# Kernel tuning notes

Measured on AMD Instinct MI355X. Metric: run time of the kernel, lower is better.

Reference implementation:

```python
import jax, jax.numpy as jnp
import numpy as np

B, T, C, H = 4, 2048, 1024, 16
HD = C // H  # head dim = 64

def setup_inputs() -> dict:
    key = jax.random.key(0)
    k1, k2, k3 = jax.random.split(key, 3)
    x = jax.random.normal(k1, (B, T, C), dtype=jnp.float32)
    w_attn = jax.random.normal(k2, (C, 3 * C), dtype=jnp.float32) * 0.02
    w_proj = jax.random.normal(k3, (C, C), dtype=jnp.float32) * 0.02
    return {"x": x, "w_attn": w_attn, "w_proj": w_proj}

def reference(x, w_attn, w_proj):
    b, t, c = x.shape
    qkv = x @ w_attn  # [B,T,3C]
    q, k, v = jnp.split(qkv, 3, axis=-1)
    # [B,T,C] -> [B,H,T,HD]
    def heads(z):
        return z.reshape(b, t, H, HD).transpose(0, 2, 1, 3)
    q, k, v = heads(q), heads(k), heads(v)
    scale = 1.0 / jnp.sqrt(jnp.float32(HD))
    att = jnp.einsum('bhqd,bhkd->bhqk', q, k) * scale  # [B,H,T,T]
    causal = jnp.tril(jnp.ones((t, t), dtype=bool))
    att = jnp.where(causal[None, None], att, -jnp.inf)
    att = jax.nn.softmax(att, axis=-1)
    y = jnp.einsum('bhqk,bhkd->bhqd', att, v)  # [B,H,T,HD]
    y = y.transpose(0, 2, 1, 3).reshape(b, t, c)
    return y @ w_proj
```

## Files before the change

### kernel.cpp

```cpp
#include <hip/hip_runtime.h>
#include <hip/hip_bf16.h>

typedef short bf16x8 __attribute__((ext_vector_type(8)));
typedef short short4v __attribute__((ext_vector_type(4)));
typedef float f32x4 __attribute__((ext_vector_type(4)));
typedef float f32x16 __attribute__((ext_vector_type(16)));

template <bool V> struct BoolC { static constexpr bool value = V; };

__device__ __forceinline__ short f2b(float f) {
  __hip_bfloat16 h = __float2bfloat16(f);
  union { __hip_bfloat16 h; short s; } u; u.h = h; return u.s;
}

__device__ __forceinline__ unsigned cvtpk_bf16(float lo, float hi) {
  unsigned r;
  asm("v_cvt_pk_bf16_f32 %0, %1, %2" : "=v"(r) : "v"(lo), "v"(hi));
  return r;
}

__device__ __forceinline__ f32x16 mfma32(bf16x8 a, bf16x8 b, f32x16 c) {
  return __builtin_amdgcn_mfma_f32_32x32x16_bf16(a, b, c, 0, 0, 0);
}

template <int N> __device__ __forceinline__ void vmwait() {
  if constexpr (N == 0) asm volatile("s_waitcnt vmcnt(0)" ::: "memory");
  else if constexpr (N == 1) asm volatile("s_waitcnt vmcnt(1)" ::: "memory");
  else if constexpr (N == 2) asm volatile("s_waitcnt vmcnt(2)" ::: "memory");
  else if constexpr (N == 3) asm volatile("s_waitcnt vmcnt(3)" ::: "memory");
  else if constexpr (N == 4) asm volatile("s_waitcnt vmcnt(4)" ::: "memory");
  else if constexpr (N == 5) asm volatile("s_waitcnt vmcnt(5)" ::: "memory");
  else if constexpr (N == 6) asm volatile("s_waitcnt vmcnt(6)" ::: "memory");
  else if constexpr (N == 7) asm volatile("s_waitcnt vmcnt(7)" ::: "memory");
  else asm volatile("s_waitcnt vmcnt(8)" ::: "memory");
}

__device__ __forceinline__ void async_copy16(const short* g, short* l) {
  __builtin_amdgcn_global_load_lds((const __attribute__((address_space(1))) void*)g,
                                   (__attribute__((address_space(3))) void*)l, 16, 0, 0);
}

__global__ __launch_bounds__(256) void pre_kernel(const float* __restrict__ x, short* __restrict__ xb,
                                                  const float* __restrict__ wa, short* __restrict__ waT,
                                                  const float* __restrict__ wp, short* __restrict__ wpT,
                                                  float qscale) {
  const int tid = threadIdx.x;
  const int blk = blockIdx.x;
  if (blk < 8192) {
    const int i = blk * 256 + tid;
    const float4 v = ((const float4*)x)[i];
    short4v o;
    o[0] = f2b(v.x); o[1] = f2b(v.y); o[2] = f2b(v.z); o[3] = f2b(v.w);
    ((short4v*)xb)[i] = o;
    return;
  }
  __shared__ float t[32][33];
  const float* in; short* out;
  int idx, gxb, Cn, qrows; float qs;
  if (blk < 11264) { idx = blk - 8192;  in = wa; out = waT; gxb = 96; Cn = 3072; qrows = 1024; qs = qscale; }
  else             { idx = blk - 11264; in = wp; out = wpT; gxb = 32; Cn = 1024; qrows = 0;    qs = 1.0f; }
  const int bx = idx % gxb, by = idx / gxb;
  const int tx = tid & 31, ty = tid >> 5;
  const int c0 = bx * 32, r0 = by * 32;
#pragma unroll
  for (int yy = 0; yy < 32; yy += 8)
    t[ty + yy][tx] = in[(size_t)(r0 + ty + yy) * Cn + (c0 + tx)];
  __syncthreads();
#pragma unroll
  for (int yy = 0; yy < 32; yy += 8) {
    const int orow = c0 + ty + yy;
    float v = t[tx][ty + yy];
    if (orow < qrows) v *= qs;
    out[(size_t)orow * 1024 + (r0 + tx)] = f2b(v);
  }
}

__global__ __launch_bounds__(256) void vtrans_kernel(const short* __restrict__ qkv,
                                                     short* __restrict__ vT) {
  constexpr int T = 2048, C3 = 3072, HD = 64;
  const int bh = blockIdx.y, b = bh >> 4, h = bh & 15;
  const int t0 = blockIdx.x * 64;
  __shared__ short tile[64][72];
  const int tid = threadIdx.x;
  const int tr = tid >> 2, dc = (tid & 3) * 16;
  const short* src = qkv + (size_t)b * T * C3 + (size_t)(t0 + tr) * C3 + 2048 + h * HD + dc;
  *(bf16x8*)&tile[tr][dc] = *(const bf16x8*)src;
  *(bf16x8*)&tile[tr][dc + 8] = *(const bf16x8*)(src + 8);
  __syncthreads();
  const int dr = tid >> 2, tc = (tid & 3) * 16;
  bf16x8 o0, o1;
#pragma unroll
  for (int i = 0; i < 8; i++) o0[i] = tile[tc + i][dr];
#pragma unroll
  for (int i = 0; i < 8; i++) o1[i] = tile[tc + 8 + i][dr];
  short* dst = vT + ((size_t)bh * HD + dr) * T + t0 + tc;
  *(bf16x8*)dst = o0;
  *(bf16x8*)(dst + 8) = o1;
}

template <int BN, typename OutT>
__global__ __launch_bounds__(256, 2) void gemm2b_kernel(const short* __restrict__ A,
                                                        const short* __restrict__ Bt,
                                                        OutT* __restrict__ C,
                                                        int M, int N, int K) {
  constexpr int NB = BN / 64;
  constexpr int NBU = BN / 32;
  constexpr int NSTREAM = NBU + 4;
  __shared__ short ldsA[2][128 * 64];
  __shared__ short ldsB[2][BN * 64];

  const int tid = threadIdx.x;
  const int w = tid >> 6, lane = tid & 63;
  const int quad = lane >> 4, l16 = lane & 15;
  const int wn = w * (BN / 4);

  const int gx = gridDim.x;
  const int nwg = gx * gridDim.y;
  const int flat = blockIdx.y * gx + blockIdx.x;
  const int swz = (flat & 7) * (nwg >> 3) + (flat >> 3);
  const int bn = swz % gx, bm = swz / gx;
  const int m0 = bm * 128, n0 = bn * BN;

  const int rsub = lane >> 3;
  const int cl = (lane & 7) ^ rsub;
  const short* pAsrc = A + (size_t)(m0 + w * 8 + rsub) * K + cl * 8;
  const short* pBsrc = Bt + (size_t)(n0 + w * 8 + rsub) * K + cl * 8;

  f32x4 acc[8][NB] = {};
  bf16x8 bfr[NB][2];

  auto issue = [&](int i, int buf, int tt) {
    if (i < NBU)
      async_copy16(pBsrc + (size_t)(i * 32) * K + tt * 64, &ldsB[buf][(i * 32 + w * 8) * 64]);
    else
      async_copy16(pAsrc + (size_t)((i - NBU) * 32) * K + tt * 64,
                   &ldsA[buf][((i - NBU) * 32 + w * 8) * 64]);
  };
  auto readA = [&](bf16x8 (&af)[2][2], int buf, int P) {
#pragma unroll
    for (int mm = 0; mm < 2; ++mm)
#pragma unroll
      for (int kh = 0; kh < 2; ++kh)
        af[mm][kh] = *(const bf16x8*)&ldsA[buf][(P * 32 + mm * 16 + l16) * 64 +
                                                (((kh * 4 + quad) ^ (l16 & 7)) * 8)];
  };
  auto readB = [&](int buf) {
#pragma unroll
    for (int nf = 0; nf < NB; ++nf)
#pragma unroll
      for (int kh = 0; kh < 2; ++kh)
        bfr[nf][kh] = *(const bf16x8*)&ldsB[buf][(wn + nf * 16 + l16) * 64 +
                                                 (((kh * 4 + quad) ^ (l16 & 7)) * 8)];
  };

#define PHASE(P)                                                                               \
  {                                                                                            \
    constexpr int ISS0 = (NSTREAM + 3) >> 2, ISS1 = (NSTREAM + 2) >> 2,                        \
                  ISS2 = (NSTREAM + 1) >> 2;                                                   \
    constexpr int CUM = ((P) > 0 ? ISS0 : 0) + ((P) > 1 ? ISS1 : 0) + ((P) > 2 ? ISS2 : 0);    \
    constexpr int GS = NSTREAM - (NBU + 1 + (P)) + CUM;                                        \
    constexpr int GL = 3 - (P);                                                                \
    if constexpr ((P) == 0) asm volatile("s_waitcnt lgkmcnt(0)" ::: "memory");                 \
    if constexpr (LAST) vmwait<GL>(); else vmwait<GS>();                                       \
    __builtin_amdgcn_s_barrier();                                                              \
    bf16x8 af[2][2];                                                                           \
    readA(af, buf, (P));                                                                       \
    if constexpr ((P) == 0) readB(buf);                                                        \
    if constexpr (!LAST) {                                                                     \
      constexpr int NI = (NSTREAM + 3 - (P)) >> 2;                                             \
      _Pragma("unroll") for (int ii = 0; ii < NI; ++ii) issue(CUM + ii, buf ^ 1, t + 1);       \
    }                                                                                          \
    __builtin_amdgcn_s_setprio(1);                                                             \
    _Pragma("unroll") for (int mm = 0; mm < 2; ++mm)                                           \
    _Pragma("unroll") for (int nf = 0; nf < NB; ++nf) {                                        \
      acc[(P)*2 + mm][nf] = __builtin_amdgcn_mfma_f32_16x16x32_bf16(af[mm][0], bfr[nf][0],     \
                                                                    acc[(P)*2 + mm][nf], 0, 0, 0); \
      acc[(P)*2 + mm][nf] = __builtin_amdgcn_mfma_f32_16x16x32_bf16(af[mm][1], bfr[nf][1],     \
                                                                    acc[(P)*2 + mm][nf], 0, 0, 0); \
    }                                                                                          \
    __builtin_amdgcn_s_setprio(0);                                                             \
  }

#pragma unroll
  for (int i = 0; i < NSTREAM; ++i) issue(i, 0, 0);

  const int NT = K >> 6;
  auto tile = [&](int t, int buf, auto lastc) {
    constexpr bool LAST = decltype(lastc)::value;
    PHASE(0)
    PHASE(1)
    PHASE(2)
    PHASE(3)
  };
  for (int t = 0; t < NT - 1; ++t) tile(t, t & 1, BoolC<false>{});
  tile(NT - 1, (NT - 1) & 1, BoolC<true>{});
#undef PHASE

  (void)M;
#pragma unroll
  for (int mf = 0; mf < 8; ++mf)
#pragma unroll
    for (int nf = 0; nf < NB; ++nf) {
      const int col = n0 + wn + nf * 16 + l16;
#pragma unroll
      for (int r = 0; r < 4; ++r) {
        const int row = m0 + mf * 16 + quad * 4 + r;
        if constexpr (sizeof(OutT) == 4)
          C[(size_t)row * N + col] = acc[mf][nf][r];
        else
          C[(size_t)row * N + col] = f2b(acc[mf][nf][r]);
      }
    }
}

__global__ __launch_bounds__(256, 2) void attn_kernel(const short* __restrict__ qkv,
                                                      const short* __restrict__ vT,
                                                      short* __restrict__ y) {
  constexpr int T = 2048, C3 = 3072, Cc = 1024, HD = 64;
  const int f = blockIdx.y * 8 + blockIdx.x;
  const int bh = (f & 7) * 8 + ((f >> 3) & 7);
  const int xb = f >> 6;
  const int b = bh >> 4, h = bh & 15;
  const int tid = threadIdx.x, lane = tid & 63, wave = tid >> 6;
  const int l32 = lane & 31, hi = lane >> 5;

  __shared__ short Ksb[2][64 * 64];
  __shared__ short Vtb[2][64 * 64];

  const size_t base = (size_t)b * T * C3;
  const int qcol = h * HD, kcol = Cc + h * HD;
  const size_t vtbase = (size_t)bh * HD * T;

  const int r8 = lane >> 3;
  const int cg8 = ((lane & 7) ^ r8) * 8;
  const short* gk[2];
  const short* gv[2];
  short* lk[2][2]; short* lv[2][2];
#pragma unroll
  for (int t8 = 0; t8 < 2; t8++) {
    const int row = wave * 16 + t8 * 8 + r8;
    gk[t8] = qkv + base + (size_t)row * C3 + kcol + cg8;
    gv[t8] = vT + vtbase + (size_t)row * T + cg8;
#pragma unroll
    for (int bu = 0; bu < 2; bu++) {
      lk[bu][t8] = &Ksb[bu][(wave * 16 + t8 * 8) * 64];
      lv[bu][t8] = &Vtb[bu][(wave * 16 + t8 * 8) * 64];
    }
  }
  const int rs7 = l32 & 7;

  bf16x8 ones;
#pragma unroll
  for (int i = 0; i < 8; i++) ones[i] = (short)0x3F80;

  for (int half = 0; half < 2; half++) {
    const int t = half ? xb : (15 - xb);
    const int q0 = t * 128;
    const int jmax = 2 * t + 1;
    const int jd = 2 * t + (wave >> 1);
    const int qrow = q0 + wave * 32 + l32;

    bf16x8 qf[4];
    {
      const short* qp = qkv + base + (size_t)qrow * C3 + qcol + hi * 8;
#pragma unroll
      for (int wk = 0; wk < 4; wk++) qf[wk] = *(const bf16x8*)(qp + wk * 16);
    }

    f32x16 o0 = {}, o1 = {}, lC = {};

    async_copy16(gk[0], lk[0][0]);
    async_copy16(gk[1], lk[0][1]);
    async_copy16(gv[0], lv[0][0]);
    async_copy16(gv[1], lv[0][1]);

    for (int j = 0; j <= jmax; j++) {
      const int cur = j & 1;
      __syncthreads();

      if (j < jmax) {
        const size_t ko = (size_t)(j + 1) * 64 * C3;
        const int vo = (j + 1) * 64;
        async_copy16(gk[0] + ko, lk[cur ^ 1][0]);
        async_copy16(gk[1] + ko, lk[cur ^ 1][1]);
        async_copy16(gv[0] + vo, lv[cur ^ 1][0]);
        async_copy16(gv[1] + vo, lv[cur ^ 1][1]);
      }

      if (j > jd) continue;

      const bool up = (64 * j + 32) <= (q0 + wave * 32 + 31);

      f32x16 st0 = {}, st1 = {};
      __builtin_amdgcn_s_setprio(1);
#pragma unroll
      for (int wk = 0; wk < 4; wk++) {
        const bf16x8 k0 = *(const bf16x8*)&Ksb[cur][l32 * 64 + (((2 * wk + hi) ^ rs7) * 8)];
        st0 = mfma32(k0, qf[wk], st0);
      }
      if (up) {
#pragma unroll
        for (int wk = 0; wk < 4; wk++) {
          const bf16x8 k1 = *(const bf16x8*)&Ksb[cur][(32 + l32) * 64 + (((2 * wk + hi) ^ rs7) * 8)];
          st1 = mfma32(k1, qf[wk], st1);
        }
      }
      __builtin_amdgcn_s_setprio(0);

      if (j == jd) {
#pragma unroll
        for (int r = 0; r < 16; r++) {
          const int kvl = 64 * j + (r & 3) + 8 * (r >> 2) + 4 * hi;
          if (kvl > qrow) st0[r] = -INFINITY;
          if (up && (kvl + 32 > qrow)) st1[r] = -INFINITY;
        }
      }

      bf16x8 vf00, vf01, vf10, vf11, vf02, vf03, vf12, vf13;
      vf00 = *(const bf16x8*)&Vtb[cur][l32 * 64 + (((0 + hi) ^ rs7) * 8)];
      vf01 = *(const bf16x8*)&Vtb[cur][l32 * 64 + (((2 + hi) ^ rs7) * 8)];
      vf10 = *(const bf16x8*)&Vtb[cur][(32 + l32) * 64 + (((0 + hi) ^ rs7) * 8)];
      vf11 = *(const bf16x8*)&Vtb[cur][(32 + l32) * 64 + (((2 + hi) ^ rs7) * 8)];
      if (up) {
        vf02 = *(const bf16x8*)&Vtb[cur][l32 * 64 + (((4 + hi) ^ rs7) * 8)];
        vf03 = *(const bf16x8*)&Vtb[cur][l32 * 64 + (((6 + hi) ^ rs7) * 8)];
        vf12 = *(const bf16x8*)&Vtb[cur][(32 + l32) * 64 + (((4 + hi) ^ rs7) * 8)];
        vf13 = *(const bf16x8*)&Vtb[cur][(32 + l32) * 64 + (((6 + hi) ^ rs7) * 8)];
      }

#pragma unroll
      for (int r = 0; r < 16; r++) st0[r] = __builtin_amdgcn_exp2f(st0[r]);
      bf16x8 pa0, pa1, pa2, pa3;
      {
        unsigned a0 = cvtpk_bf16(st0[0], st0[1]), c0 = cvtpk_bf16(st0[2], st0[3]);
        unsigned b0 = cvtpk_bf16(st0[4], st0[5]), d0 = cvtpk_bf16(st0[6], st0[7]);
        asm volatile("v_permlane32_swap_b32 %0, %1" : "+v"(a0), "+v"(b0));
        asm volatile("v_permlane32_swap_b32 %0, %1" : "+v"(c0), "+v"(d0));
        union { unsigned u[4]; bf16x8 v; } p; p.u[0] = a0; p.u[1] = c0; p.u[2] = b0; p.u[3] = d0;
        pa0 = p.v;
        unsigned a1 = cvtpk_bf16(st0[8], st0[9]), c1 = cvtpk_bf16(st0[10], st0[11]);
        unsigned b1 = cvtpk_bf16(st0[12], st0[13]), d1 = cvtpk_bf16(st0[14], st0[15]);
        asm volatile("v_permlane32_swap_b32 %0, %1" : "+v"(a1), "+v"(b1));
        asm volatile("v_permlane32_swap_b32 %0, %1" : "+v"(c1), "+v"(d1));
        union { unsigned u[4]; bf16x8 v; } q; q.u[0] = a1; q.u[1] = c1; q.u[2] = b1; q.u[3] = d1;
        pa1 = q.v;
      }
      if (up) {
#pragma unroll
        for (int r = 0; r < 16; r++) st1[r] = __builtin_amdgcn_exp2f(st1[r]);
        unsigned a2 = cvtpk_bf16(st1[0], st1[1]), c2 = cvtpk_bf16(st1[2], st1[3]);
        unsigned b2 = cvtpk_bf16(st1[4], st1[5]), d2 = cvtpk_bf16(st1[6], st1[7]);
        asm volatile("v_permlane32_swap_b32 %0, %1" : "+v"(a2), "+v"(b2));
        asm volatile("v_permlane32_swap_b32 %0, %1" : "+v"(c2), "+v"(d2));
        union { unsigned u[4]; bf16x8 v; } p; p.u[0] = a2; p.u[1] = c2; p.u[2] = b2; p.u[3] = d2;
        pa2 = p.v;
        unsigned a3 = cvtpk_bf16(st1[8], st1[9]), c3 = cvtpk_bf16(st1[10], st1[11]);
        unsigned b3 = cvtpk_bf16(st1[12], st1[13]), d3 = cvtpk_bf16(st1[14], st1[15]);
        asm volatile("v_permlane32_swap_b32 %0, %1" : "+v"(a3), "+v"(b3));
        asm volatile("v_permlane32_swap_b32 %0, %1" : "+v"(c3), "+v"(d3));
        union { unsigned u[4]; bf16x8 v; } q; q.u[0] = a3; q.u[1] = c3; q.u[2] = b3; q.u[3] = d3;
        pa3 = q.v;
      }

      __builtin_amdgcn_s_setprio(1);
      lC = mfma32(pa0, ones, lC);
      lC = mfma32(pa1, ones, lC);
      o0 = mfma32(pa0, vf00, o0);
      o0 = mfma32(pa1, vf01, o0);
      o1 = mfma32(pa0, vf10, o1);
      o1 = mfma32(pa1, vf11, o1);
      if (up) {
        lC = mfma32(pa2, ones, lC);
        lC = mfma32(pa3, ones, lC);
        o0 = mfma32(pa2, vf02, o0);
        o0 = mfma32(pa3, vf03, o0);
        o1 = mfma32(pa2, vf12, o1);
        o1 = mfma32(pa3, vf13, o1);
      }
      __builtin_amdgcn_s_setprio(0);
    }

#pragma unroll
    for (int r = 0; r < 16; r++) {
      const int rq = (r & 3) + 8 * (r >> 2) + 4 * hi;
      const int row_g = q0 + wave * 32 + rq;
      const float inv = 1.0f / lC[r];
      short* yp = y + (size_t)(b * T + row_g) * Cc + h * HD;
      yp[l32] = f2b(o0[r] * inv);
      yp[32 + l32] = f2b(o1[r] * inv);
    }
  }
}

extern "C" void kernel_launch(void* const* d_in, const int* in_sizes, int n_in,
                              void* d_out, int out_size, void* d_ws, size_t ws_size,
                              hipStream_t stream) {
  constexpr int B = 4, T = 2048, C = 1024;
  constexpr int M = B * T;
  constexpr int N1 = 3 * C;
  const float* x      = (const float*)d_in[0];
  const float* w_attn = (const float*)d_in[1];
  const float* w_proj = (const float*)d_in[2];
  float* out = (float*)d_out;

  char* ws = (char*)d_ws;
  short* xb   = (short*)(ws + 0);
  short* waT  = (short*)(ws + 16777216);
  short* wpT  = (short*)(ws + 23068672);
  short* qkvb = (short*)(ws + 25165824);
  short* yb   = (short*)(ws + 75497472);
  short* vT   = xb;

  const float qscale = 0.125f * 1.44269504088896340736f;

  pre_kernel<<<12288, 256, 0, stream>>>(x, xb, w_attn, waT, w_proj, wpT, qscale);
  gemm2b_kernel<192, short><<<dim3(N1 / 192, M / 128), 256, 0, stream>>>(xb, waT, qkvb, M, N1, C);
  vtrans_kernel<<<dim3(T / 64, B * 16), 256, 0, stream>>>(qkvb, vT);
  attn_kernel<<<dim3(8, B * 16), 256, 0, stream>>>(qkvb, vT, yb);
  gemm2b_kernel<128, float><<<dim3(C / 128, M / 128), 256, 0, stream>>>(yb, wpT, out, M, C, C);
}
```

Before: 226.8 us.

## Halve attention block to 64 query rows with two waves and padded LDS tiles

The attention kernel now launches 1024 blocks of 128 threads, each handling a 64-row query tile, instead of 512 blocks of 256 threads handling 128 rows. This aims at finer causal load balancing, since the paired-tile scheme now uses 32 tiles per head and fewer waves sit idle on diagonal blocks. The K/V shared tiles gain 8 elements of padding per 8-row group to change bank mapping. Each wave now issues twice as many async copies per tile, and the extra blocks add barrier and launch overhead.

```diff
diff --git a/kernel.cpp b/kernel.cpp
--- a/kernel.cpp
+++ b/kernel.cpp
@@ -213,19 +213,19 @@
     }
 }
 
-__global__ __launch_bounds__(256, 2) void attn_kernel(const short* __restrict__ qkv,
+__global__ __launch_bounds__(128, 2) void attn_kernel(const short* __restrict__ qkv,
                                                       const short* __restrict__ vT,
                                                       short* __restrict__ y) {
   constexpr int T = 2048, C3 = 3072, Cc = 1024, HD = 64;
-  const int f = blockIdx.y * 8 + blockIdx.x;
+  const int f = blockIdx.y * 16 + blockIdx.x;
   const int bh = (f & 7) * 8 + ((f >> 3) & 7);
   const int xb = f >> 6;
   const int b = bh >> 4, h = bh & 15;
   const int tid = threadIdx.x, lane = tid & 63, wave = tid >> 6;
   const int l32 = lane & 31, hi = lane >> 5;
 
-  __shared__ short Ksb[2][64 * 64];
-  __shared__ short Vtb[2][64 * 64];
+  __shared__ short Ksb[2][4160];
+  __shared__ short Vtb[2][4160];
 
   const size_t base = (size_t)b * T * C3;
   const int qcol = h * HD, kcol = Cc + h * HD;
@@ -233,31 +233,33 @@
 
   const int r8 = lane >> 3;
   const int cg8 = ((lane & 7) ^ r8) * 8;
-  const short* gk[2];
-  const short* gv[2];
-  short* lk[2][2]; short* lv[2][2];
-#pragma unroll
-  for (int t8 = 0; t8 < 2; t8++) {
-    const int row = wave * 16 + t8 * 8 + r8;
-    gk[t8] = qkv + base + (size_t)row * C3 + kcol + cg8;
-    gv[t8] = vT + vtbase + (size_t)row * T + cg8;
+  const short* gk[4];
+  const short* gv[4];
+  short* lk[2][4]; short* lv[2][4];
+#pragma unroll
+  for (int i = 0; i < 4; i++) {
+    const int g = wave * 4 + i;
+    const int row = g * 8 + r8;
+    gk[i] = qkv + base + (size_t)row * C3 + kcol + cg8;
+    gv[i] = vT + vtbase + (size_t)row * T + cg8;
 #pragma unroll
     for (int bu = 0; bu < 2; bu++) {
-      lk[bu][t8] = &Ksb[bu][(wave * 16 + t8 * 8) * 64];
-      lv[bu][t8] = &Vtb[bu][(wave * 16 + t8 * 8) * 64];
+      lk[bu][i] = &Ksb[bu][g * 520];
+      lv[bu][i] = &Vtb[bu][g * 520];
     }
   }
   const int rs7 = l32 & 7;
+  const int rb0 = (l32 >> 3) * 520 + rs7 * 64;
+  const int rb1 = (4 + (l32 >> 3)) * 520 + rs7 * 64;
 
   bf16x8 ones;
 #pragma unroll
   for (int i = 0; i < 8; i++) ones[i] = (short)0x3F80;
 
   for (int half = 0; half < 2; half++) {
-    const int t = half ? xb : (15 - xb);
-    const int q0 = t * 128;
-    const int jmax = 2 * t + 1;
-    const int jd = 2 * t + (wave >> 1);
+    const int t = half ? xb : (31 - xb);
+    const int q0 = t * 64;
+    const int jmax = t;
     const int qrow = q0 + wave * 32 + l32;
 
     bf16x8 qf[4];
@@ -269,10 +271,12 @@
 
     f32x16 o0 = {}, o1 = {}, lC = {};
 
-    async_copy16(gk[0], lk[0][0]);
-    async_copy16(gk[1], lk[0][1]);
-    async_copy16(gv[0], lv[0][0]);
-    async_copy16(gv[1], lv[0][1]);
+    __syncthreads();
+
+#pragma unroll
+    for (int i = 0; i < 4; i++) async_copy16(gk[i], lk[0][i]);
+#pragma unroll
+    for (int i = 0; i < 4; i++) async_copy16(gv[i], lv[0][i]);
 
     for (int j = 0; j <= jmax; j++) {
       const int cur = j & 1;
@@ -281,51 +285,56 @@
       if (j < jmax) {
         const size_t ko = (size_t)(j + 1) * 64 * C3;
         const int vo = (j + 1) * 64;
-        async_copy16(gk[0] + ko, lk[cur ^ 1][0]);
-        async_copy16(gk[1] + ko, lk[cur ^ 1][1]);
-        async_copy16(gv[0] + vo, lv[cur ^ 1][0]);
-        async_copy16(gv[1] + vo, lv[cur ^ 1][1]);
-      }
-
-      if (j > jd) continue;
-
-      const bool up = (64 * j + 32) <= (q0 + wave * 32 + 31);
+#pragma unroll
+        for (int i = 0; i < 4; i++) async_copy16(gk[i] + ko, lk[cur ^ 1][i]);
+#pragma unroll
+        for (int i = 0; i < 4; i++) async_copy16(gv[i] + vo, lv[cur ^ 1][i]);
+      }
+
+      const bool up = (j < jmax) || (wave == 1);
 
       f32x16 st0 = {}, st1 = {};
       __builtin_amdgcn_s_setprio(1);
 #pragma unroll
       for (int wk = 0; wk < 4; wk++) {
-        const bf16x8 k0 = *(const bf16x8*)&Ksb[cur][l32 * 64 + (((2 * wk + hi) ^ rs7) * 8)];
+        const bf16x8 k0 = *(const bf16x8*)&Ksb[cur][rb0 + (((2 * wk + hi) ^ rs7) * 8)];
         st0 = mfma32(k0, qf[wk], st0);
       }
       if (up) {
 #pragma unroll
         for (int wk = 0; wk < 4; wk++) {
-          const bf16x8 k1 = *(const bf16x8*)&Ksb[cur][(32 + l32) * 64 + (((2 * wk + hi) ^ rs7) * 8)];
+          const bf16x8 k1 = *(const bf16x8*)&Ksb[cur][rb1 + (((2 * wk + hi) ^ rs7) * 8)];
           st1 = mfma32(k1, qf[wk], st1);
         }
       }
       __builtin_amdgcn_s_setprio(0);
 
-      if (j == jd) {
-#pragma unroll
-        for (int r = 0; r < 16; r++) {
-          const int kvl = 64 * j + (r & 3) + 8 * (r >> 2) + 4 * hi;
-          if (kvl > qrow) st0[r] = -INFINITY;
-          if (up && (kvl + 32 > qrow)) st1[r] = -INFINITY;
+      if (j == jmax) {
+        if (!up) {
+#pragma unroll
+          for (int r = 0; r < 16; r++) {
+            const int kvl = 64 * j + (r & 3) + 8 * (r >> 2) + 4 * hi;
+            if (kvl > qrow) st0[r] = -INFINITY;
+          }
+        } else {
+#pragma unroll
+          for (int r = 0; r < 16; r++) {
+            const int kvl = 64 * j + (r & 3) + 8 * (r >> 2) + 4 * hi + 32;
+            if (kvl > qrow) st1[r] = -INFINITY;
+          }
         }
       }
 
       bf16x8 vf00, vf01, vf10, vf11, vf02, vf03, vf12, vf13;
-      vf00 = *(const bf16x8*)&Vtb[cur][l32 * 64 + (((0 + hi) ^ rs7) * 8)];
-      vf01 = *(const bf16x8*)&Vtb[cur][l32 * 64 + (((2 + hi) ^ rs7) * 8)];
-      vf10 = *(const bf16x8*)&Vtb[cur][(32 + l32) * 64 + (((0 + hi) ^ rs7) * 8)];
-      vf11 = *(const bf16x8*)&Vtb[cur][(32 + l32) * 64 + (((2 + hi) ^ rs7) * 8)];
+      vf00 = *(const bf16x8*)&Vtb[cur][rb0 + (((0 + hi) ^ rs7) * 8)];
+      vf01 = *(const bf16x8*)&Vtb[cur][rb0 + (((2 + hi) ^ rs7) * 8)];
+      vf10 = *(const bf16x8*)&Vtb[cur][rb1 + (((0 + hi) ^ rs7) * 8)];
+      vf11 = *(const bf16x8*)&Vtb[cur][rb1 + (((2 + hi) ^ rs7) * 8)];
       if (up) {
-        vf02 = *(const bf16x8*)&Vtb[cur][l32 * 64 + (((4 + hi) ^ rs7) * 8)];
-        vf03 = *(const bf16x8*)&Vtb[cur][l32 * 64 + (((6 + hi) ^ rs7) * 8)];
-        vf12 = *(const bf16x8*)&Vtb[cur][(32 + l32) * 64 + (((4 + hi) ^ rs7) * 8)];
-        vf13 = *(const bf16x8*)&Vtb[cur][(32 + l32) * 64 + (((6 + hi) ^ rs7) * 8)];
+        vf02 = *(const bf16x8*)&Vtb[cur][rb0 + (((4 + hi) ^ rs7) * 8)];
+        vf03 = *(const bf16x8*)&Vtb[cur][rb0 + (((6 + hi) ^ rs7) * 8)];
+        vf12 = *(const bf16x8*)&Vtb[cur][rb1 + (((4 + hi) ^ rs7) * 8)];
+        vf13 = *(const bf16x8*)&Vtb[cur][rb1 + (((6 + hi) ^ rs7) * 8)];
       }
 
 #pragma unroll
@@ -416,6 +425,6 @@
   pre_kernel<<<12288, 256, 0, stream>>>(x, xb, w_attn, waT, w_proj, wpT, qscale);
   gemm2b_kernel<192, short><<<dim3(N1 / 192, M / 128), 256, 0, stream>>>(xb, waT, qkvb, M, N1, C);
   vtrans_kernel<<<dim3(T / 64, B * 16), 256, 0, stream>>>(qkvb, vT);
-  attn_kernel<<<dim3(8, B * 16), 256, 0, stream>>>(qkvb, vT, yb);
+  attn_kernel<<<dim3(16, B * 16), 128, 0, stream>>>(qkvb, vT, yb);
   gemm2b_kernel<128, float><<<dim3(C / 128, M / 128), 256, 0, stream>>>(yb, wpT, out, M, C, C);
 }
```

Result: slower. 232.1 us (+2.4%).
